# Optimization experiments

Measured on AMD Instinct MI355X. Metric: run time of the kernel, lower is better.

Reference implementation:

```python
import jax, jax.numpy as jnp
import numpy as np

D_MODEL, D_STATE, D_CONV, D_INNER = 1024, 16, 4, 2048
BATCH, SEQLEN = 4, 2048


def setup_inputs() -> dict:
    key = jax.random.key(0)
    ks = jax.random.split(key, 8)
    x = jax.random.normal(ks[0], (BATCH, SEQLEN, D_MODEL), jnp.float32)
    W_in = jax.random.normal(ks[1], (D_MODEL, 2 * D_INNER), jnp.float32) / np.float32(np.sqrt(D_MODEL))
    conv_w = jax.random.normal(ks[2], (D_INNER, 1, D_CONV), jnp.float32) * np.float32(0.3)
    W_x = jax.random.normal(ks[3], (D_INNER, 2 * D_STATE), jnp.float32) / np.float32(np.sqrt(D_INNER))
    W_dt = jax.random.normal(ks[4], (D_STATE, D_INNER), jnp.float32) / np.float32(np.sqrt(D_STATE))
    b_dt = jax.random.normal(ks[5], (D_INNER,), jnp.float32) * np.float32(0.1)
    W_Bp = jax.random.normal(ks[6], (D_STATE, D_INNER), jnp.float32) / np.float32(np.sqrt(D_STATE))
    D_param = jnp.ones((D_INNER,), jnp.float32)
    W_out = jax.random.normal(ks[7], (D_INNER, D_MODEL), jnp.float32) / np.float32(np.sqrt(D_INNER))
    return {"x": x, "W_in": W_in, "conv_w": conv_w, "W_x": W_x,
            "W_dt": W_dt, "b_dt": b_dt, "W_Bp": W_Bp, "D_param": D_param,
            "W_out": W_out}


def _mamba_fwd(x, W_in, conv_w, W_x, W_dt, b_dt, W_Bp, D_param, W_out):
    B, L, _ = x.shape
    xz = x @ W_in                                   # [B,L,2*d_inner]
    xc, z = jnp.split(xz, 2, axis=-1)
    # causal depthwise conv1d (torch pads d_conv-1 both sides then slices [:L])
    xt = jnp.transpose(xc, (0, 2, 1))               # [B,d_inner,L]
    xt = jax.lax.conv_general_dilated(
        xt, conv_w,
        window_strides=(1,), padding=[(D_CONV - 1, 0)],
        dimension_numbers=("NCH", "OIH", "NCH"),
        feature_group_count=D_INNER)
    u = jax.nn.silu(jnp.transpose(xt, (0, 2, 1)))   # [B,L,d_inner]
    xp = u @ W_x                                    # [B,L,2*d_state]
    dt_raw, B_raw = jnp.split(xp, 2, axis=-1)
    dt = jax.nn.softplus(dt_raw @ W_dt + b_dt)      # [B,L,d_inner]
    Bp = B_raw @ W_Bp                               # [B,L,d_inner]
    dt = jnp.clip(dt, 1e-4, 1.0)
    # selective scan: h_t = h_{t-1}*(1-dt_t) + u_t*Bp_t (note: A is unused in source)
    ub = u * Bp
    def step(h, inp):
        d_t, ub_t = inp
        h = h * (1.0 - d_t) + ub_t
        return h, h
    _, ys = jax.lax.scan(step, jnp.zeros((B, D_INNER), x.dtype),
                         (jnp.transpose(dt, (1, 0, 2)), jnp.transpose(ub, (1, 0, 2))))
    y = jnp.transpose(ys, (1, 0, 2)) + D_param * u  # [B,L,d_inner]
    y = y * jax.nn.silu(z)
    return y @ W_out                                # [B,L,d_model]


def reference(x, W_in, conv_w, W_x, W_dt, b_dt, W_Bp, D_param, W_out):
    # dropout is identity in eval mode
    return _mamba_fwd(x, W_in, conv_w, W_x, W_dt, b_dt, W_Bp, D_param, W_out)
```

## Files before the change

### kernel.cpp

```cpp
#include <hip/hip_runtime.h>
#include <cstdint>
#include <cstddef>

#define DM   1024
#define DI   2048
#define SEQ  2048
#define NB   4
#define NTOK (NB*SEQ)
#define CCH  32
#define LC   (SEQ/CCH)
#define KS   8

typedef __attribute__((ext_vector_type(8))) short short8v;
typedef __attribute__((ext_vector_type(4))) float f32x4;
typedef unsigned short u16;
typedef unsigned int   u32;

__device__ __forceinline__ float silu_f(float x){ return x / (1.f + __expf(-x)); }

__device__ __forceinline__ float softplus_f(float x){
  return (x > 20.f) ? x : __logf(1.f + __expf(x));
}

__device__ __forceinline__ u16 f2bf(float f){
  union { float f; u32 u; } c; c.f = f;
  u32 u = c.u + 0x7FFFu + ((c.u >> 16) & 1u);
  return (u16)(u >> 16);
}
__device__ __forceinline__ float b2f(u16 b){
  union { u32 u; float f; } c; c.u = ((u32)b) << 16; return c.f;
}
__device__ __forceinline__ float lo2f(u32 v){ union { u32 u; float f; } c; c.u = v << 16; return c.f; }
__device__ __forceinline__ float hi2f(u32 v){ union { u32 u; float f; } c; c.u = v & 0xFFFF0000u; return c.f; }
__device__ __forceinline__ u32 pack2(float a, float b){ return (u32)f2bf(a) | ((u32)f2bf(b) << 16); }

__device__ __forceinline__ void gl16(const void* g, void* l){
  __builtin_amdgcn_global_load_lds((const __attribute__((address_space(1))) void*)g,
                                   (__attribute__((address_space(3))) void*)l, 16, 0, 0);
}

#define PREP_CVT   8192
#define PREP_T1    (PREP_CVT + 1024)
#define PREP_T2    (PREP_T1 + 512)
#define PREP_TOTAL (PREP_T2 + 768)

__device__ void transcvt_dev(const float* __restrict__ W, u16* __restrict__ Wt,
                             int R, int Cn, int bx, int by, int tid,
                             float (*t)[65])
{
  const int lr4 = tid >> 6;
  const int lc  = tid & 63;
  #pragma unroll
  for (int p = 0; p < 16; ++p) {
    int lr = p * 4 + lr4;
    t[lr][lc] = W[(size_t)(by * 64 + lr) * Cn + bx * 64 + lc];
  }
  __syncthreads();
  #pragma unroll
  for (int p = 0; p < 16; ++p) {
    int orr = p * 4 + lr4;
    Wt[(size_t)(bx * 64 + orr) * R + by * 64 + lc] = f2bf(t[lc][orr]);
  }
}

__global__ __launch_bounds__(256) void prep_all(
    const float* __restrict__ x, u16* __restrict__ xbf,
    const float* __restrict__ W_in, u16* __restrict__ wtib,
    const float* __restrict__ W_out, u16* __restrict__ wtob,
    const float* __restrict__ W_x, const float* __restrict__ W_dt,
    const float* __restrict__ W_Bp, u16* __restrict__ Wxt, u16* __restrict__ Wbig)
{
  __shared__ float t[64][65];
  const int bid = blockIdx.x, tid = threadIdx.x;
  if (bid < PREP_CVT) {
    int i = bid * 256 + tid;
    float4 v = ((const float4*)x)[i];
    *(uint2*)(xbf + (size_t)i * 4) = make_uint2(pack2(v.x, v.y), pack2(v.z, v.w));
  } else if (bid < PREP_T1) {
    int r = bid - PREP_CVT;
    transcvt_dev(W_in, wtib, DM, 2 * DI, r & 63, r >> 6, tid, t);
  } else if (bid < PREP_T2) {
    int r = bid - PREP_T1;
    transcvt_dev(W_out, wtob, DI, DM, r & 15, r >> 4, tid, t);
  } else {
    int i = (bid - PREP_T2) * 256 + tid;
    if (i < 32 * DI) {
      int j = i >> 11, c = i & (DI - 1);
      Wxt[i] = f2bf(W_x[c * 32 + j]);
    }
    int i2 = i - 32 * DI;
    if (i2 >= 0 && i2 < 2 * DI * 32) {
      int n = i2 >> 5, k = i2 & 31;
      float v;
      if (n < DI) v = (k < 16) ? W_dt[k * DI + n] : 0.f;
      else        v = (k >= 16) ? W_Bp[(k - 16) * DI + (n - DI)] : 0.f;
      Wbig[i2] = f2bf(v);
    }
  }
}

template<int NT, int OBF16>
__global__ __launch_bounds__(256, 2) void gemm2b(
    const u16* __restrict__ A, const u16* __restrict__ Bt,
    void* C0v, void* C1v, int K, int split, int ldc)
{
  __shared__ __align__(16) u16 Ab[2][128 * 64];
  __shared__ __align__(16) u16 Bb[2][128 * 64];
  const int tid = threadIdx.x, lane = tid & 63, w = tid >> 6;
  const int wm = w >> 1, wn = w & 1;
  const int bm = blockIdx.y * 128, bn = blockIdx.x * 128;

  const int srow8 = tid >> 3;
  const int kc = ((tid & 7) ^ (srow8 & 7)) << 3;
  const u16* Ag = A  + (size_t)(bm + srow8) * K + kc;
  const u16* Bg = Bt + (size_t)(bn + srow8) * K + kc;

  const int lq = lane >> 4, l15 = lane & 15;
  const int co0 = ((lq    ) ^ (l15 & 7)) << 3;
  const int co1 = ((lq + 4) ^ (l15 & 7)) << 3;
  const int abase = (wm * 64 + l15) * 64;
  const int bbase = (wn * 64 + l15) * 64;

  f32x4 acc[4][4] = {};

  auto issue = [&](int t, int buf) {
    const size_t k0 = (size_t)t << 6;
    #pragma unroll
    for (int q = 0; q < 4; ++q)
      gl16(Ag + (size_t)(q * 32) * K + k0, &Ab[buf][q * 2048 + tid * 8]);
    #pragma unroll
    for (int q = 0; q < 4; ++q)
      gl16(Bg + (size_t)(q * 32) * K + k0, &Bb[buf][q * 2048 + tid * 8]);
  };
  auto compute = [&](int buf) {
    const u16* Ac = Ab[buf];
    const u16* Bc = Bb[buf];
    short8v af[4], bf[4];
    #pragma unroll
    for (int ks = 0; ks < 2; ++ks) {
      const int co = ks ? co1 : co0;
      #pragma unroll
      for (int i = 0; i < 4; ++i) af[i] = *(const short8v*)&Ac[abase + i * 1024 + co];
      #pragma unroll
      for (int j = 0; j < 4; ++j) bf[j] = *(const short8v*)&Bc[bbase + j * 1024 + co];
      __builtin_amdgcn_s_setprio(1);
      #pragma unroll
      for (int i = 0; i < 4; ++i)
        #pragma unroll
        for (int j = 0; j < 4; ++j)
          acc[i][j] = __builtin_amdgcn_mfma_f32_16x16x32_bf16(af[i], bf[j], acc[i][j], 0, 0, 0);
      __builtin_amdgcn_s_setprio(0);
    }
  };

  issue(0, 0); issue(1, 1);
  #pragma unroll 1
  for (int t = 0; t < NT; ++t) {
    if (t + 1 < NT) asm volatile("s_waitcnt vmcnt(8)" ::: "memory");
    else            asm volatile("s_waitcnt vmcnt(0)" ::: "memory");
    __builtin_amdgcn_s_barrier(); __builtin_amdgcn_sched_barrier(0);
    compute(t & 1);
    __builtin_amdgcn_s_barrier(); __builtin_amdgcn_sched_barrier(0);
    if (t + 2 < NT) issue(t + 2, t & 1);
  }

  const bool left = (bn < split);
  const int cb = bn - (left ? 0 : split) + wn * 64 + l15;
  const int rb = bm + wm * 64 + lq * 4;
  if (OBF16) {
    u16* Cp = (u16*)(left ? C0v : C1v);
    #pragma unroll
    for (int i = 0; i < 4; ++i)
      #pragma unroll
      for (int j = 0; j < 4; ++j)
        #pragma unroll
        for (int r = 0; r < 4; ++r)
          Cp[(size_t)(rb + i * 16 + r) * ldc + cb + j * 16] = f2bf(acc[i][j][r]);
  } else {
    float* Cp = (float*)(left ? C0v : C1v);
    #pragma unroll
    for (int i = 0; i < 4; ++i)
      #pragma unroll
      for (int j = 0; j < 4; ++j)
        #pragma unroll
        for (int r = 0; r < 4; ++r)
          Cp[(size_t)(rb + i * 16 + r) * ldc + cb + j * 16] = acc[i][j][r];
  }
}

__global__ __launch_bounds__(256) void xp_gemm(
    const u16* __restrict__ A, const u16* __restrict__ Bt, float* __restrict__ xpp)
{
  __shared__ __align__(16) u16 Asm[128 * 32];
  __shared__ __align__(16) u16 Bsm[32 * 32];
  const int tid = threadIdx.x, lane = tid & 63, w = tid >> 6;
  const int bm = blockIdx.x * 128;
  const int kbase = blockIdx.y * (DI / KS);
  f32x4 acc[2][2] = {};
  const int srow = w * 32 + (lane >> 2);
  const int soct = lane & 3;
  const u16* Ap = A + (size_t)(bm + srow) * DI + kbase + soct * 8;
  const u16* Bp = Bt + (size_t)(lane >> 2) * DI + kbase + soct * 8;
  u16* As0 = &Asm[w * 1024];

  for (int k0 = 0; k0 < DI / KS; k0 += 32) {
    gl16(Ap + k0,                      As0);
    gl16(Ap + k0 + (size_t)16 * DI,    As0 + 512);
    if (w == 0) {
      gl16(Bp + k0,                    Bsm);
      gl16(Bp + k0 + (size_t)16 * DI,  Bsm + 512);
    }
    __syncthreads();
    short8v af[2], bf[2];
    #pragma unroll
    for (int i = 0; i < 2; ++i)
      af[i] = *(const short8v*)&Asm[(w * 32 + i * 16 + (lane & 15)) * 32 + (lane >> 4) * 8];
    #pragma unroll
    for (int j = 0; j < 2; ++j)
      bf[j] = *(const short8v*)&Bsm[(j * 16 + (lane & 15)) * 32 + (lane >> 4) * 8];
    #pragma unroll
    for (int i = 0; i < 2; ++i)
      #pragma unroll
      for (int j = 0; j < 2; ++j)
        acc[i][j] = __builtin_amdgcn_mfma_f32_16x16x32_bf16(af[i], bf[j], acc[i][j], 0, 0, 0);
    __syncthreads();
  }
  float* op = xpp + (size_t)blockIdx.y * NTOK * 32;
  const int rb = bm + w * 32 + (lane >> 4) * 4;
  const int cb = lane & 15;
  #pragma unroll
  for (int i = 0; i < 2; ++i)
    #pragma unroll
    for (int j = 0; j < 2; ++j)
      #pragma unroll
      for (int r = 0; r < 4; ++r)
        op[(size_t)(rb + i * 16 + r) * 32 + cb + j * 16] = acc[i][j][r];
}

__global__ __launch_bounds__(256) void xp_reduce(
    const float* __restrict__ xpp, u16* __restrict__ xpb)
{
  int i = blockIdx.x * 256 + threadIdx.x;
  float s = 0.f;
  #pragma unroll
  for (int k = 0; k < KS; ++k) s += xpp[(size_t)k * NTOK * 32 + i];
  xpb[i] = f2bf(s);
}

__global__ __launch_bounds__(256) void dtub_scan(
    const u16* __restrict__ A,
    const u16* __restrict__ Bt,
    const float* __restrict__ b_dt, const u16* __restrict__ u,
    u16* __restrict__ dt_out, u16* __restrict__ ub_out,
    float* __restrict__ P, float* __restrict__ S)
{
  __shared__ __align__(16) u16 smem[32768];
  u16* Asm = smem;
  u16* Bsm = smem + 4096;
  const int tid = threadIdx.x, lane = tid & 63, w = tid >> 6;
  const int wm = w >> 1, wn = w & 1;
  const int bm = blockIdx.y * 128, bc = blockIdx.x * 128;
  const int srow = w * 32 + (lane >> 2);
  const int soct = lane & 3;
  u16* As0 = Asm + w * 1024;
  u16* Bs0 = Bsm + w * 1024;
  u16* Bs1 = Bsm + 4096 + w * 1024;
  gl16(A  + (size_t)(bm + srow) * 32 + soct * 8,            As0);
  gl16(A  + (size_t)(bm + srow) * 32 + soct * 8 + 512,      As0 + 512);
  gl16(Bt + (size_t)(bc + srow) * 32 + soct * 8,            Bs0);
  gl16(Bt + (size_t)(bc + srow) * 32 + soct * 8 + 512,      Bs0 + 512);
  gl16(Bt + (size_t)(DI + bc + srow) * 32 + soct * 8,       Bs1);
  gl16(Bt + (size_t)(DI + bc + srow) * 32 + soct * 8 + 512, Bs1 + 512);
  __syncthreads();

  const int lq = lane >> 4, l15 = lane & 15;
  f32x4 accd[4][4] = {}, accu[4][4] = {};
  short8v afr[4], bfd[4], bfu[4];
  #pragma unroll
  for (int i = 0; i < 4; ++i) {
    afr[i] = *(const short8v*)&Asm[(wm * 64 + i * 16 + l15) * 32 + lq * 8];
    bfd[i] = *(const short8v*)&Bsm[(wn * 64 + i * 16 + l15) * 32 + lq * 8];
    bfu[i] = *(const short8v*)&Bsm[4096 + (wn * 64 + i * 16 + l15) * 32 + lq * 8];
  }
  #pragma unroll
  for (int i = 0; i < 4; ++i)
    #pragma unroll
    for (int j = 0; j < 4; ++j) {
      accd[i][j] = __builtin_amdgcn_mfma_f32_16x16x32_bf16(afr[i], bfd[j], accd[i][j], 0, 0, 0);
      accu[i][j] = __builtin_amdgcn_mfma_f32_16x16x32_bf16(afr[i], bfu[j], accu[i][j], 0, 0, 0);
    }
  __syncthreads();
  u16* dtL = smem;
  u16* ubL = smem + 16384;

  const int rl = wm * 64 + lq * 4;
  const int cl = wn * 64 + l15;
  float bd[4];
  #pragma unroll
  for (int j = 0; j < 4; ++j) bd[j] = b_dt[bc + cl + j * 16];
  #pragma unroll
  for (int i = 0; i < 4; ++i)
    #pragma unroll
    for (int j = 0; j < 4; ++j)
      #pragma unroll
      for (int r = 0; r < 4; ++r) {
        const int row = rl + i * 16 + r, col = cl + j * 16;
        const size_t off = (size_t)(bm + row) * DI + bc + col;
        float sp = softplus_f(accd[i][j][r] + bd[j]);
        sp = fminf(fmaxf(sp, 1e-4f), 1.0f);
        u16 dv = f2bf(sp);
        u16 uv = f2bf(b2f(u[off]) * accu[i][j][r]);
        dt_out[off] = dv; dtL[row * 128 + col] = dv;
        ub_out[off] = uv; ubL[row * 128 + col] = uv;
      }
  __syncthreads();

  {
    const int chunk = tid >> 7, ch = tid & 127;
    float p = 1.f, s = 0.f;
    #pragma unroll 4
    for (int t = 0; t < LC; ++t) {
      int rr = chunk * LC + t;
      float a = 1.f - b2f(dtL[rr * 128 + ch]);
      s = s * a + b2f(ubL[rr * 128 + ch]);
      p *= a;
    }
    const int gt = (bm >> 6) + chunk;
    P[(size_t)gt * DI + bc + ch] = p;
    S[(size_t)gt * DI + bc + ch] = s;
  }
}

__global__ __launch_bounds__(256) void conv_silu_k(
    const u16* __restrict__ xc, const float* __restrict__ cw, u16* __restrict__ u)
{
  int idx = blockIdx.x * 256 + threadIdx.x;
  int c = (idx & (DI / 4 - 1)) << 2;
  int r = idx >> 9;
  int t = r & (SEQ - 1);
  float4 w0 = ((const float4*)cw)[c + 0];
  float4 w1 = ((const float4*)cw)[c + 1];
  float4 w2 = ((const float4*)cw)[c + 2];
  float4 w3 = ((const float4*)cw)[c + 3];
  const u16* base = xc + (size_t)r * DI + c;
  uint2 v = *(const uint2*)base;
  float a0 = w0.w * lo2f(v.x), a1 = w1.w * hi2f(v.x);
  float a2 = w2.w * lo2f(v.y), a3 = w3.w * hi2f(v.y);
  if (t >= 1) { v = *(const uint2*)(base - DI);
    a0 += w0.z * lo2f(v.x); a1 += w1.z * hi2f(v.x); a2 += w2.z * lo2f(v.y); a3 += w3.z * hi2f(v.y); }
  if (t >= 2) { v = *(const uint2*)(base - 2 * DI);
    a0 += w0.y * lo2f(v.x); a1 += w1.y * hi2f(v.x); a2 += w2.y * lo2f(v.y); a3 += w3.y * hi2f(v.y); }
  if (t >= 3) { v = *(const uint2*)(base - 3 * DI);
    a0 += w0.x * lo2f(v.x); a1 += w1.x * hi2f(v.x); a2 += w2.x * lo2f(v.y); a3 += w3.x * hi2f(v.y); }
  *(uint2*)(u + (size_t)r * DI + c) =
      make_uint2(pack2(silu_f(a0), silu_f(a1)), pack2(silu_f(a2), silu_f(a3)));
}

__global__ __launch_bounds__(256) void scan_p2(
    const float* __restrict__ P, const float* __restrict__ S, float* __restrict__ Hin)
{
  int idx = blockIdx.x * 256 + threadIdx.x;
  int di = idx & (DI - 1);
  int b  = idx >> 11;
  float h = 0.f;
  #pragma unroll
  for (int c = 0; c < CCH; ++c) {
    size_t off = ((size_t)b * CCH + c) * DI + di;
    Hin[off] = h;
    h = h * P[off] + S[off];
  }
}

__global__ __launch_bounds__(256) void scan_p3(
    const u16* dt_, const u16* __restrict__ ub, const u16* __restrict__ u,
    const u16* __restrict__ z, const float* __restrict__ Dp_,
    const float* __restrict__ Hin, u16* y)
{
  int idx = blockIdx.x * 256 + threadIdx.x;
  int di = (idx & (DI / 4 - 1)) << 2;
  int bc = idx >> 9;
  int c  = bc & (CCH - 1);
  int b  = bc >> 5;
  float4 dp = ((const float4*)Dp_)[di >> 2];
  float4 h4 = ((const float4*)Hin)[idx];
  float h0 = h4.x, h1 = h4.y, h2 = h4.z, h3 = h4.w;
  size_t base = ((size_t)b * SEQ + (size_t)c * LC) * DI + di;
  #pragma unroll 4
  for (int t = 0; t < LC; ++t) {
    size_t off = base + (size_t)t * DI;
    uint2 dv = *(const uint2*)(dt_ + off);
    uint2 uv = *(const uint2*)(ub + off);
    uint2 uu = *(const uint2*)(u + off);
    uint2 zv = *(const uint2*)(z + off);
    h0 = h0 * (1.f - lo2f(dv.x)) + lo2f(uv.x);
    h1 = h1 * (1.f - hi2f(dv.x)) + hi2f(uv.x);
    h2 = h2 * (1.f - lo2f(dv.y)) + lo2f(uv.y);
    h3 = h3 * (1.f - hi2f(dv.y)) + hi2f(uv.y);
    float y0 = (h0 + dp.x * lo2f(uu.x)) * silu_f(lo2f(zv.x));
    float y1 = (h1 + dp.y * hi2f(uu.x)) * silu_f(hi2f(zv.x));
    float y2 = (h2 + dp.z * lo2f(uu.y)) * silu_f(lo2f(zv.y));
    float y3 = (h3 + dp.w * hi2f(uu.y)) * silu_f(hi2f(zv.y));
    *(uint2*)(y + off) = make_uint2(pack2(y0, y1), pack2(y2, y3));
  }
}

extern "C" void kernel_launch(void* const* d_in, const int* in_sizes, int n_in,
                              void* d_out, int out_size, void* d_ws, size_t ws_size,
                              hipStream_t stream)
{
  const float* x     = (const float*)d_in[0];
  const float* W_in  = (const float*)d_in[1];
  const float* cw    = (const float*)d_in[2];
  const float* W_x   = (const float*)d_in[3];
  const float* W_dt  = (const float*)d_in[4];
  const float* b_dt  = (const float*)d_in[5];
  const float* W_Bp  = (const float*)d_in[6];
  const float* Dp    = (const float*)d_in[7];
  const float* W_out = (const float*)d_in[8];
  float* out = (float*)d_out;

  const size_t SZ = (size_t)NTOK * DI;
  float* w    = (float*)d_ws;
  float* bufA = w;
  float* bufB = w + SZ;
  float* bufC = w + 2 * SZ;
  float* bufD = w + 3 * SZ;

  u16* xcb  = (u16*)bufA;
  u16* zb   = (u16*)bufB;
  u16* wtob = zb + (size_t)NTOK * DI;
  u16* wxt  = wtob + (size_t)DM * DI;
  u16* wbig = wxt + (size_t)32 * DI;
  u16* xbf  = (u16*)bufC;
  u16* wtib = xbf + (size_t)NTOK * DM;
  u16* ubf  = (u16*)bufC;
  u16* ubb  = (u16*)bufD;

  const size_t PS = (size_t)NB * CCH * DI;
  float* Pbuf   = out;
  float* Sbuf   = out + PS;
  float* Hin    = out + 2 * PS;
  float* xppart = out + 3 * PS;
  u16*   xpb    = (u16*)(out + 3 * PS + (size_t)KS * NTOK * 32);
  (void)ws_size; (void)in_sizes; (void)n_in; (void)out_size;

  prep_all<<<PREP_TOTAL, 256, 0, stream>>>(
      x, xbf, W_in, wtib, W_out, wtob, W_x, W_dt, W_Bp, wxt, wbig);

  gemm2b<DM / 64, 1><<<dim3((2 * DI) / 128, NTOK / 128), 256, 0, stream>>>(
      xbf, wtib, (void*)xcb, (void*)zb, DM, DI, DI);

  conv_silu_k<<<(NTOK * DI / 4) / 256, 256, 0, stream>>>(xcb, cw, ubf);

  xp_gemm<<<dim3(NTOK / 128, KS), 256, 0, stream>>>(ubf, wxt, xppart);
  xp_reduce<<<(NTOK * 32) / 256, 256, 0, stream>>>(xppart, xpb);
  dtub_scan<<<dim3(DI / 128, NTOK / 128), 256, 0, stream>>>(
      xpb, wbig, b_dt, ubf, xcb, ubb, Pbuf, Sbuf);

  scan_p2<<<(NB * DI) / 256, 256, 0, stream>>>(Pbuf, Sbuf, Hin);
  scan_p3<<<(NB * CCH * DI / 4) / 256, 256, 0, stream>>>(xcb, ubb, ubf, zb, Dp, Hin, xcb);

  gemm2b<DI / 64, 0><<<dim3(DM / 128, NTOK / 128), 256, 0, stream>>>(
      xcb, wtob, (void*)out, (void*)out, DI, DM, DM);
}
```

Before: 281.5 us.

## Add triple-buffered 64x256-tile GEMM kernel for output projection

Replaces the generic gemm2b kernel for the final y@W_out projection with a new gemm2n kernel. It uses 64x256 tiles, a three-stage async global-to-LDS pipeline with explicit vmcnt waits, XOR-swizzled LDS layout to avoid bank conflicts, and s_setprio around the MFMA block. The goal is to hide load latency and raise MFMA utilization. The trade-offs are more LDS per block (two blocks per CU) and a different grid shape, which could affect occupancy or tail effects.

```diff
diff --git a/kernel.cpp b/kernel.cpp
--- a/kernel.cpp
+++ b/kernel.cpp
@@ -188,6 +188,76 @@
   }
 }
 
+template<int NT>
+__global__ __launch_bounds__(256, 2) void gemm2n(
+    const u16* __restrict__ A, const u16* __restrict__ Bt,
+    float* __restrict__ C, int K, int ldc)
+{
+  __shared__ __align__(16) u16 Ab[3][64 * 32];
+  __shared__ __align__(16) u16 Bb[3][256 * 32];
+  const int tid = threadIdx.x, lane = tid & 63, w = tid >> 6;
+  const int bm = blockIdx.y * 64, bn = blockIdx.x * 256;
+
+  const int srow = tid >> 2;
+  const int kc = ((tid & 3) ^ ((srow >> 1) & 3)) << 3;
+  const u16* Ag = A  + (size_t)(bm + srow) * K + kc;
+  const u16* Bg = Bt + (size_t)(bn + srow) * K + kc;
+
+  const int lq = lane >> 4, l15 = lane & 15;
+  const int co = (lq ^ ((l15 >> 1) & 3)) << 3;
+  const int bbase = (w * 64 + l15) * 32;
+
+  f32x4 acc[4][4] = {};
+
+  auto issue = [&](int t, int buf) {
+    const size_t k0 = (size_t)t << 5;
+    gl16(Ag + k0, &Ab[buf][tid * 8]);
+    #pragma unroll
+    for (int q = 0; q < 4; ++q)
+      gl16(Bg + (size_t)(q * 64) * K + k0, &Bb[buf][q * 2048 + tid * 8]);
+  };
+  auto compute = [&](int buf) {
+    const u16* Ac = Ab[buf];
+    const u16* Bc = Bb[buf];
+    short8v af[4], bf[4];
+    #pragma unroll
+    for (int i = 0; i < 4; ++i) af[i] = *(const short8v*)&Ac[(i * 16 + l15) * 32 + co];
+    #pragma unroll
+    for (int j = 0; j < 4; ++j) bf[j] = *(const short8v*)&Bc[bbase + j * 512 + co];
+    __builtin_amdgcn_s_setprio(1);
+    #pragma unroll
+    for (int i = 0; i < 4; ++i)
+      #pragma unroll
+      for (int j = 0; j < 4; ++j)
+        acc[i][j] = __builtin_amdgcn_mfma_f32_16x16x32_bf16(af[i], bf[j], acc[i][j], 0, 0, 0);
+    __builtin_amdgcn_s_setprio(0);
+  };
+
+  issue(0, 0); issue(1, 1); issue(2, 2);
+  int cur = 0;
+  #pragma unroll 1
+  for (int t = 0; t < NT; ++t) {
+    if (t + 2 < NT)      asm volatile("s_waitcnt vmcnt(10)" ::: "memory");
+    else if (t + 1 < NT) asm volatile("s_waitcnt vmcnt(5)"  ::: "memory");
+    else                 asm volatile("s_waitcnt vmcnt(0)"  ::: "memory");
+    __builtin_amdgcn_s_barrier(); __builtin_amdgcn_sched_barrier(0);
+    compute(cur);
+    __builtin_amdgcn_s_barrier(); __builtin_amdgcn_sched_barrier(0);
+    if (t + 3 < NT) issue(t + 3, cur);
+    cur = (cur == 2) ? 0 : cur + 1;
+  }
+
+  const int rb = bm + lq * 4;
+  const int cb = bn + w * 64 + l15;
+  #pragma unroll
+  for (int i = 0; i < 4; ++i)
+    #pragma unroll
+    for (int j = 0; j < 4; ++j)
+      #pragma unroll
+      for (int r = 0; r < 4; ++r)
+        C[(size_t)(rb + i * 16 + r) * ldc + cb + j * 16] = acc[i][j][r];
+}
+
 __global__ __launch_bounds__(256) void xp_gemm(
     const u16* __restrict__ A, const u16* __restrict__ Bt, float* __restrict__ xpp)
 {
@@ -460,6 +530,6 @@
   scan_p2<<<(NB * DI) / 256, 256, 0, stream>>>(Pbuf, Sbuf, Hin);
   scan_p3<<<(NB * CCH * DI / 4) / 256, 256, 0, stream>>>(xcb, ubb, ubf, zb, Dp, Hin, xcb);
 
-  gemm2b<DI / 64, 0><<<dim3(DM / 128, NTOK / 128), 256, 0, stream>>>(
-      xcb, wtob, (void*)out, (void*)out, DI, DM, DM);
-}
+  gemm2n<DI / 32><<<dim3(DM / 256, NTOK / 64), 256, 0, stream>>>(
+      xcb, wtob, out, DI, DM);
+}
```

Measured after the change: 304.3 us. 8.1% more time.
